# Kernel optimization log

Measured on AMD Instinct MI355X. Metric: run time of the kernel, lower is better.

Reference implementation:

```python
import jax, jax.numpy as jnp
import numpy as np

H_IMG, W_IMG = 1024, 1280
MAX_ITER = 3
DAMPING = 1e-6
DIST_THR = 0.2
NORM_THR = float(np.cos(np.deg2rad(20.0)))


def setup_inputs() -> dict:
    key = jax.random.key(0)
    k1, k2, k3, k4 = jax.random.split(key, 4)
    H, W = H_IMG, W_IMG
    fx = fy = 1000.0
    cx, cy = (W - 1) / 2.0, (H - 1) / 2.0
    K = jnp.array([[fx, 0.0, cx], [0.0, fy, cy], [0.0, 0.0, 1.0]], dtype=jnp.float32)
    # backproject a random depth map so vertex maps are geometrically consistent with K
    depth = 0.5 + 2.5 * jax.random.uniform(k1, (H, W), dtype=jnp.float32)
    vv, uu = jnp.meshgrid(jnp.arange(H, dtype=jnp.float32), jnp.arange(W, dtype=jnp.float32), indexing='ij')
    vertex_t0 = jnp.stack([(uu - cx) / fx * depth, (vv - cy) / fy * depth, depth], axis=-1)
    n = jax.random.normal(k2, (H, W, 3), dtype=jnp.float32) * 0.1 + jnp.array([0.0, 0.0, -1.0], jnp.float32)
    normal_t0 = n / jnp.linalg.norm(n, axis=-1, keepdims=True)
    # frame 1 = slightly perturbed frame 0 (realistic small-motion ICP)
    vertex_t1 = vertex_t0 + 0.002 * jax.random.normal(k3, (H, W, 3), dtype=jnp.float32)
    n1 = normal_t0 + 0.01 * jax.random.normal(k4, (H, W, 3), dtype=jnp.float32)
    normal_t1 = n1 / jnp.linalg.norm(n1, axis=-1, keepdims=True)
    pose10 = jnp.eye(4, dtype=jnp.float32).at[:3, 3].set(jnp.array([0.005, -0.003, 0.002], jnp.float32))
    return {
        'pose10': pose10,
        'vertex_t0': vertex_t0.astype(jnp.float32),
        'vertex_t1': vertex_t1.astype(jnp.float32),
        'normal_t0': normal_t0.astype(jnp.float32),
        'normal_t1': normal_t1.astype(jnp.float32),
        'K': K,
    }


def _skew3(w):
    o = jnp.zeros((), w.dtype)
    return jnp.array([[o, -w[2], w[1]], [w[2], o, -w[0]], [-w[1], w[0], o]])


def _exp_se3(xi):
    w, v = xi[:3], xi[3:6]
    wh = _skew3(w)
    wh2 = wh @ wh
    theta = jnp.linalg.norm(w)
    eps = 1e-8
    ts = jnp.maximum(theta, eps)  # safe denominator
    sin_t, cos_t = jnp.sin(ts), jnp.cos(ts)
    eye3 = jnp.eye(3, dtype=xi.dtype)
    e_w_big = eye3 + wh * (sin_t / ts) + wh2 * ((1.0 - cos_t) / ts ** 2)
    j_big = eye3 + ((1.0 - cos_t) / ts ** 2) * wh + ((ts - sin_t) / ts ** 3) * wh2
    small = theta <= eps
    e_w = jnp.where(small, eye3, e_w_big)
    j = jnp.where(small, eye3, j_big)
    return jnp.eye(4, dtype=xi.dtype).at[:3, :3].set(e_w).at[:3, 3].set(j @ v)


def _warp_nearest(feat, u, v):
    # grid_sample(mode='nearest', padding='border', align_corners=True) with
    # the module's normalization reduces to nearest-pixel gather at (v,u), clamped.
    H, W, _ = feat.shape
    ui = jnp.clip(jnp.round(u), 0, W - 1).astype(jnp.int32)
    vi = jnp.clip(jnp.round(v), 0, H - 1).astype(jnp.int32)
    return feat[vi, ui]  # (H,W,C)


def _icp_step(pose, vertex0, vertex1, normal0, normal1, mask0, K):
    R, t = pose[:3, :3], pose[:3, 3]
    H, W, _ = vertex0.shape
    p = vertex0 @ R.T + t          # vertex0_to1, (H,W,3)
    n0 = normal0 @ R.T             # normal0_to1
    fx, fy, cx, cy = K[0, 0], K[1, 1], K[0, 2], K[1, 2]
    z = p[..., 2]
    u = p[..., 0] / z * fx + cx
    v = p[..., 1] / z * fy + cy
    inview = (u > 0) & (u < W - 1) & (v > 0) & (v < H - 1)
    rv1 = _warp_nearest(vertex1, u, v)
    rn1 = _warp_nearest(normal1, u, v)
    mask1 = rv1[..., -1] > 0.0
    diff = p - rv1
    normal_ok = jnp.sum(n0 * rn1, axis=-1) > NORM_THR
    res = jnp.sum(rn1 * diff, axis=-1)           # (H,W)
    # -n^T skew(p) == cross(p, n)
    J = jnp.concatenate([jnp.cross(p, rn1), rn1], axis=-1)  # (H,W,6)
    occ = (~inview) | (jnp.linalg.norm(diff, axis=-1) > DIST_THR)
    invalid = occ | (~mask0) | (~mask1) | (~normal_ok)
    J = jnp.where(invalid[..., None], 0.0, J).reshape(-1, 6)
    r = jnp.where(invalid, 0.0, res).reshape(-1)
    JtJ = J.T @ J                                 # (6,6)
    JtR = J.T @ r                                 # (6,)
    Hm = JtJ + jnp.trace(JtJ) * DAMPING * jnp.eye(6, dtype=JtJ.dtype)
    xi = -(jnp.linalg.inv(Hm) @ JtR)
    return _exp_se3(xi) @ pose, ~invalid


def reference(pose10, vertex_t0, vertex_t1, normal_t0, normal_t1, K):
    mask0 = vertex_t0[..., -1] > 0.0
    pose = pose10
    valid = None
    for _ in range(MAX_ITER):
        pose, valid = _icp_step(pose, vertex_t0, vertex_t1, normal_t0, normal_t1, mask0, K)
    H, W = vertex_t0.shape[:2]
    valid_ratio = valid.astype(jnp.float32).sum() / H / W
    return pose, valid_ratio
```

## Files before the change

kernel.cpp:

```cpp
#include <hip/hip_runtime.h>
#include <math.h>

#define H_IMG 1024
#define W_IMG 1280
#define NPIX (H_IMG * W_IMG)
#define NQUAD (NPIX / 4)
#define RBLOCKS 256
#define RTPB 256
#define QPT (NQUAD / (RBLOCKS * RTPB))
#define NACC 28
#define NORM_THR 0.93969262f
#define DIST_THR2 0.04f
#define DAMPING 1e-6

#define PART_DOUBLES (RBLOCKS * NACC)

__global__ __launch_bounds__(256) void icp_init(const float* __restrict__ pose_in,
                                                double* __restrict__ ws) {
    const int i = threadIdx.x;
    if (i < 16) ws[i] = (double)pose_in[i];
    for (int k = i; k < PART_DOUBLES; k += 256) ws[16 + k] = 0.0;
    if (i == 0) *(unsigned*)(ws + 16 + PART_DOUBLES) = 0u;
}

__device__ void solve_and_update(const double* tot, double* pose_ws,
                                 float* out, int write_out) {
    double JtJ[6][6];
    {
        int k = 0;
        for (int i = 0; i < 6; ++i)
            for (int j = i; j < 6; ++j) { JtJ[i][j] = tot[k]; JtJ[j][i] = tot[k]; ++k; }
    }
    double tr = 0.0;
    for (int i = 0; i < 6; ++i) tr += JtJ[i][i];

    double A[6][7];
    for (int i = 0; i < 6; ++i) {
        for (int j = 0; j < 6; ++j) A[i][j] = JtJ[i][j] + (i == j ? tr * DAMPING : 0.0);
        A[i][6] = -tot[21 + i];
    }
    for (int c = 0; c < 6; ++c) {
        int piv = c; double mx = fabs(A[c][c]);
        for (int r = c + 1; r < 6; ++r) {
            double ar = fabs(A[r][c]);
            if (ar > mx) { mx = ar; piv = r; }
        }
        if (piv != c) for (int j = 0; j < 7; ++j) { double tmp = A[c][j]; A[c][j] = A[piv][j]; A[piv][j] = tmp; }
        double d = A[c][c]; if (d == 0.0) d = 1e-30;
        for (int r = c + 1; r < 6; ++r) {
            double f = A[r][c] / d;
            for (int j = c; j < 7; ++j) A[r][j] -= f * A[c][j];
        }
    }
    double xi[6];
    for (int i = 5; i >= 0; --i) {
        double s = A[i][6];
        for (int j = i + 1; j < 6; ++j) s -= A[i][j] * xi[j];
        double d = A[i][i]; if (d == 0.0) d = 1e-30;
        xi[i] = s / d;
    }

    const double w0 = xi[0], w1 = xi[1], w2 = xi[2];
    const double v0 = xi[3], v1 = xi[4], v2 = xi[5];
    double wh[3][3] = { {0.0, -w2, w1}, {w2, 0.0, -w0}, {-w1, w0, 0.0} };
    double wh2[3][3];
    for (int i = 0; i < 3; ++i)
        for (int j = 0; j < 3; ++j) {
            double s = 0.0;
            for (int k = 0; k < 3; ++k) s += wh[i][k] * wh[k][j];
            wh2[i][j] = s;
        }
    const double theta = sqrt(w0 * w0 + w1 * w1 + w2 * w2);
    const double eps = 1e-8;
    const double ts = (theta > eps) ? theta : eps;
    const double st = sin(ts), ct = cos(ts);
    const double cA = st / ts;
    const double cB = (1.0 - ct) / (ts * ts);
    const double cC = (ts - st) / (ts * ts * ts);
    const bool small = (theta <= eps);

    double ew[3][3], Jm[3][3];
    for (int i = 0; i < 3; ++i)
        for (int j = 0; j < 3; ++j) {
            double eye = (i == j) ? 1.0 : 0.0;
            ew[i][j] = small ? eye : (eye + cA * wh[i][j] + cB * wh2[i][j]);
            Jm[i][j] = small ? eye : (eye + cB * wh[i][j] + cC * wh2[i][j]);
        }
    double Jv[3];
    for (int i = 0; i < 3; ++i) Jv[i] = Jm[i][0] * v0 + Jm[i][1] * v1 + Jm[i][2] * v2;

    double T[16] = { ew[0][0], ew[0][1], ew[0][2], Jv[0],
                     ew[1][0], ew[1][1], ew[1][2], Jv[1],
                     ew[2][0], ew[2][1], ew[2][2], Jv[2],
                     0.0, 0.0, 0.0, 1.0 };
    double P[16];
    for (int i = 0; i < 16; ++i) P[i] = pose_ws[i];
    double NP[16];
    for (int i = 0; i < 4; ++i)
        for (int j = 0; j < 4; ++j) {
            double s = 0.0;
            for (int k = 0; k < 4; ++k) s += T[i * 4 + k] * P[k * 4 + j];
            NP[i * 4 + j] = s;
        }
    for (int i = 0; i < 16; ++i) pose_ws[i] = NP[i];

    if (write_out) {
        for (int i = 0; i < 16; ++i) out[i] = (float)NP[i];
        out[16] = (float)(tot[27] / (double)NPIX);
    }
}

__global__ __launch_bounds__(RTPB, 1) void icp_fused(
    const float* __restrict__ vert0, const float* __restrict__ vert1,
    const float* __restrict__ norm0, const float* __restrict__ norm1,
    const float* __restrict__ Kmat, double* __restrict__ ws,
    float* __restrict__ out, int write_out)
{
    const double* pose = ws;
    double* part = ws + 16;
    unsigned* counter = (unsigned*)(ws + 16 + PART_DOUBLES);

    const float R00 = (float)pose[0],  R01 = (float)pose[1],  R02 = (float)pose[2],  t0 = (float)pose[3];
    const float R10 = (float)pose[4],  R11 = (float)pose[5],  R12 = (float)pose[6],  t1 = (float)pose[7];
    const float R20 = (float)pose[8],  R21 = (float)pose[9],  R22 = (float)pose[10], t2 = (float)pose[11];
    const float fx = Kmat[0], cx = Kmat[2], fy = Kmat[4], cy = Kmat[5];

    float a[NACC];
#pragma unroll
    for (int k = 0; k < NACC; ++k) a[k] = 0.0f;

    const int tid0 = blockIdx.x * RTPB + threadIdx.x;
    const float4* v0q = (const float4*)vert0;
    const float4* n0q = (const float4*)norm0;

    float4 cA0, cA1, cA2, cB0, cB1, cB2;
    {
        const int q = tid0;
        cA0 = v0q[q * 3 + 0]; cA1 = v0q[q * 3 + 1]; cA2 = v0q[q * 3 + 2];
        cB0 = n0q[q * 3 + 0]; cB1 = n0q[q * 3 + 1]; cB2 = n0q[q * 3 + 2];
    }

#pragma unroll
    for (int i = 0; i < QPT; ++i) {
        const float vx[4] = {cA0.x, cA0.w, cA1.z, cA2.y};
        const float vy[4] = {cA0.y, cA1.x, cA1.w, cA2.z};
        const float vz[4] = {cA0.z, cA1.y, cA2.x, cA2.w};
        const float nx[4] = {cB0.x, cB0.w, cB1.z, cB2.y};
        const float ny[4] = {cB0.y, cB1.x, cB1.w, cB2.z};
        const float nz[4] = {cB0.z, cB1.y, cB2.x, cB2.w};

        float px[4], py[4], pz[4], nrx[4], nry[4], nrz[4];
        bool inview[4];
        int wb[4];
#pragma unroll
        for (int p = 0; p < 4; ++p) {
            px[p] = R00 * vx[p] + R01 * vy[p] + R02 * vz[p] + t0;
            py[p] = R10 * vx[p] + R11 * vy[p] + R12 * vz[p] + t1;
            pz[p] = R20 * vx[p] + R21 * vy[p] + R22 * vz[p] + t2;
            nrx[p] = R00 * nx[p] + R01 * ny[p] + R02 * nz[p];
            nry[p] = R10 * nx[p] + R11 * ny[p] + R12 * nz[p];
            nrz[p] = R20 * nx[p] + R21 * ny[p] + R22 * nz[p];
            const float u = px[p] / pz[p] * fx + cx;
            const float v = py[p] / pz[p] * fy + cy;
            inview[p] = (u > 0.0f) && (u < (float)(W_IMG - 1)) &&
                        (v > 0.0f) && (v < (float)(H_IMG - 1));
            const float uf = fminf(fmaxf(rintf(u), 0.0f), (float)(W_IMG - 1));
            const float vf = fminf(fmaxf(rintf(v), 0.0f), (float)(H_IMG - 1));
            wb[p] = ((int)vf * W_IMG + (int)uf) * 3;
        }

        float r1x[4], r1y[4], r1z[4], m1x[4], m1y[4], m1z[4];
#pragma unroll
        for (int p = 0; p < 4; ++p) {
            r1x[p] = vert1[wb[p]]; r1y[p] = vert1[wb[p] + 1]; r1z[p] = vert1[wb[p] + 2];
            m1x[p] = norm1[wb[p]]; m1y[p] = norm1[wb[p] + 1]; m1z[p] = norm1[wb[p] + 2];
        }

        float4 nA0, nA1, nA2, nB0, nB1, nB2;
        if (i + 1 < QPT) {
            const int q = tid0 + (i + 1) * (RBLOCKS * RTPB);
            nA0 = v0q[q * 3 + 0]; nA1 = v0q[q * 3 + 1]; nA2 = v0q[q * 3 + 2];
            nB0 = n0q[q * 3 + 0]; nB1 = n0q[q * 3 + 1]; nB2 = n0q[q * 3 + 2];
        }

#pragma unroll
        for (int p = 0; p < 4; ++p) {
            const float dx = px[p] - r1x[p], dy = py[p] - r1y[p], dz = pz[p] - r1z[p];
            const bool mask0 = vz[p] > 0.0f;
            const bool mask1 = r1z[p] > 0.0f;
            const bool normal_ok =
                (nrx[p] * m1x[p] + nry[p] * m1y[p] + nrz[p] * m1z[p]) > NORM_THR;
            const float d2 = dx * dx + dy * dy + dz * dz;
            const bool occ = (!inview[p]) || (d2 > DIST_THR2);
            const bool valid = (!occ) && mask0 && mask1 && normal_ok;

            if (valid) {
                const float res = m1x[p] * dx + m1y[p] * dy + m1z[p] * dz;
                float J[6];
                J[0] = py[p] * m1z[p] - pz[p] * m1y[p];
                J[1] = pz[p] * m1x[p] - px[p] * m1z[p];
                J[2] = px[p] * m1y[p] - py[p] * m1x[p];
                J[3] = m1x[p]; J[4] = m1y[p]; J[5] = m1z[p];
                int k = 0;
#pragma unroll
                for (int ii = 0; ii < 6; ++ii)
#pragma unroll
                    for (int jj = ii; jj < 6; ++jj) a[k++] += J[ii] * J[jj];
#pragma unroll
                for (int ii = 0; ii < 6; ++ii) a[21 + ii] += J[ii] * res;
                a[27] += 1.0f;
            }
        }

        if (i + 1 < QPT) {
            cA0 = nA0; cA1 = nA1; cA2 = nA2;
            cB0 = nB0; cB1 = nB1; cB2 = nB2;
        }
    }

#pragma unroll
    for (int k = 0; k < NACC; ++k) {
        float val = a[k];
        for (int off = 32; off > 0; off >>= 1) val += __shfl_down(val, off, 64);
        a[k] = val;
    }

    __shared__ float sh[4][NACC];
    const int lane = threadIdx.x & 63;
    const int wid  = threadIdx.x >> 6;
    if (lane == 0) {
#pragma unroll
        for (int k = 0; k < NACC; ++k) sh[wid][k] = a[k];
    }
    __syncthreads();

    const unsigned tid = threadIdx.x;
    if (tid < NACC) {
        double s = (double)sh[0][tid] + (double)sh[1][tid] +
                   (double)sh[2][tid] + (double)sh[3][tid];
        __hip_atomic_store(&part[blockIdx.x * NACC + (int)tid], s,
                           __ATOMIC_RELAXED, __HIP_MEMORY_SCOPE_AGENT);
    }
    __syncthreads();

    __shared__ bool amLast;
    if (tid == 0) {
        __threadfence();
        unsigned prev = atomicAdd(counter, 1u);
        amLast = (prev == gridDim.x - 1);
    }
    __syncthreads();

    if (amLast) {
        __threadfence();
        __shared__ double red[8][NACC];
        __shared__ double tot[NACC];
        const int k = (int)tid % NACC;
        const int g = (int)tid / NACC;
        if (tid < 8 * NACC) {
            double s = 0.0;
#pragma unroll
            for (int b = 0; b < RBLOCKS / 8; ++b) {
                const int blk = g + b * 8;
                s += __hip_atomic_load(&part[blk * NACC + k],
                                       __ATOMIC_RELAXED, __HIP_MEMORY_SCOPE_AGENT);
            }
            red[g][k] = s;
        }
        __syncthreads();
        if (tid < NACC) {
            double s = 0.0;
#pragma unroll
            for (int g2 = 0; g2 < 8; ++g2) s += red[g2][tid];
            tot[tid] = s;
        }
        __syncthreads();
        if (tid == 0) {
            solve_and_update(tot, ws, out, write_out);
            atomicExch(counter, 0u);
        }
    }
}

extern "C" void kernel_launch(void* const* d_in, const int* in_sizes, int n_in,
                              void* d_out, int out_size, void* d_ws, size_t ws_size,
                              hipStream_t stream) {
    const float* pose10 = (const float*)d_in[0];
    const float* vert0  = (const float*)d_in[1];
    const float* vert1  = (const float*)d_in[2];
    const float* norm0  = (const float*)d_in[3];
    const float* norm1  = (const float*)d_in[4];
    const float* Kmat   = (const float*)d_in[5];
    float* out = (float*)d_out;
    double* ws = (double*)d_ws;

    icp_init<<<1, 256, 0, stream>>>(pose10, ws);
    for (int it = 0; it < 3; ++it) {
        icp_fused<<<RBLOCKS, RTPB, 0, stream>>>(vert0, vert1, norm0, norm1,
                                                Kmat, ws, out, it == 2 ? 1 : 0);
    }
}
```

Before: 209.9 us.

## Stride pixels across grid per thread, swizzle block IDs, read initial pose directly

Each thread now handles pixels strided by the whole grid, loaded as scalar xyz triples, where before it read contiguous quads through float4 loads. Block indices are swizzled across groups of eight. The init kernel is reduced to clearing the counter, and the first iteration reads the input pose directly instead of a copied workspace pose. The aim is to give neighbouring threads more coherent gather locations in vert1/norm1 and to cut init work, at the cost of losing the wide float4 loads for the streamed inputs.

```diff
diff --git a/kernel.cpp b/kernel.cpp
--- a/kernel.cpp
+++ b/kernel.cpp
@@ -4,10 +4,12 @@
 #define H_IMG 1024
 #define W_IMG 1280
 #define NPIX (H_IMG * W_IMG)
-#define NQUAD (NPIX / 4)
 #define RBLOCKS 256
 #define RTPB 256
-#define QPT (NQUAD / (RBLOCKS * RTPB))
+#define NWAVES (RTPB / 64)
+#define STRIDE (RBLOCKS * RTPB)
+#define PPT (NPIX / STRIDE)
+#define GROUPS (PPT / 4)
 #define NACC 28
 #define NORM_THR 0.93969262f
 #define DIST_THR2 0.04f
@@ -15,15 +17,12 @@
 
 #define PART_DOUBLES (RBLOCKS * NACC)
 
-__global__ __launch_bounds__(256) void icp_init(const float* __restrict__ pose_in,
-                                                double* __restrict__ ws) {
-    const int i = threadIdx.x;
-    if (i < 16) ws[i] = (double)pose_in[i];
-    for (int k = i; k < PART_DOUBLES; k += 256) ws[16 + k] = 0.0;
-    if (i == 0) *(unsigned*)(ws + 16 + PART_DOUBLES) = 0u;
+__global__ void icp_init0(double* __restrict__ ws) {
+    if (threadIdx.x == 0) *(unsigned*)(ws + 16 + PART_DOUBLES) = 0u;
 }
 
 __device__ void solve_and_update(const double* tot, double* pose_ws,
+                                 const float* pose_in, int it,
                                  float* out, int write_out) {
     double JtJ[6][6];
     {
@@ -94,7 +93,7 @@
                      ew[2][0], ew[2][1], ew[2][2], Jv[2],
                      0.0, 0.0, 0.0, 1.0 };
     double P[16];
-    for (int i = 0; i < 16; ++i) P[i] = pose_ws[i];
+    for (int i = 0; i < 16; ++i) P[i] = (it == 0) ? (double)pose_in[i] : pose_ws[i];
     double NP[16];
     for (int i = 0; i < 4; ++i)
         for (int j = 0; j < 4; ++j) {
@@ -110,113 +109,12 @@
     }
 }
 
-__global__ __launch_bounds__(RTPB, 1) void icp_fused(
-    const float* __restrict__ vert0, const float* __restrict__ vert1,
-    const float* __restrict__ norm0, const float* __restrict__ norm1,
-    const float* __restrict__ Kmat, double* __restrict__ ws,
-    float* __restrict__ out, int write_out)
+__device__ __forceinline__ void reduce_and_finish(
+    float a[NACC], double* ws, const float* pose_in, int it,
+    float* out, int write_out)
 {
-    const double* pose = ws;
     double* part = ws + 16;
     unsigned* counter = (unsigned*)(ws + 16 + PART_DOUBLES);
-
-    const float R00 = (float)pose[0],  R01 = (float)pose[1],  R02 = (float)pose[2],  t0 = (float)pose[3];
-    const float R10 = (float)pose[4],  R11 = (float)pose[5],  R12 = (float)pose[6],  t1 = (float)pose[7];
-    const float R20 = (float)pose[8],  R21 = (float)pose[9],  R22 = (float)pose[10], t2 = (float)pose[11];
-    const float fx = Kmat[0], cx = Kmat[2], fy = Kmat[4], cy = Kmat[5];
-
-    float a[NACC];
-#pragma unroll
-    for (int k = 0; k < NACC; ++k) a[k] = 0.0f;
-
-    const int tid0 = blockIdx.x * RTPB + threadIdx.x;
-    const float4* v0q = (const float4*)vert0;
-    const float4* n0q = (const float4*)norm0;
-
-    float4 cA0, cA1, cA2, cB0, cB1, cB2;
-    {
-        const int q = tid0;
-        cA0 = v0q[q * 3 + 0]; cA1 = v0q[q * 3 + 1]; cA2 = v0q[q * 3 + 2];
-        cB0 = n0q[q * 3 + 0]; cB1 = n0q[q * 3 + 1]; cB2 = n0q[q * 3 + 2];
-    }
-
-#pragma unroll
-    for (int i = 0; i < QPT; ++i) {
-        const float vx[4] = {cA0.x, cA0.w, cA1.z, cA2.y};
-        const float vy[4] = {cA0.y, cA1.x, cA1.w, cA2.z};
-        const float vz[4] = {cA0.z, cA1.y, cA2.x, cA2.w};
-        const float nx[4] = {cB0.x, cB0.w, cB1.z, cB2.y};
-        const float ny[4] = {cB0.y, cB1.x, cB1.w, cB2.z};
-        const float nz[4] = {cB0.z, cB1.y, cB2.x, cB2.w};
-
-        float px[4], py[4], pz[4], nrx[4], nry[4], nrz[4];
-        bool inview[4];
-        int wb[4];
-#pragma unroll
-        for (int p = 0; p < 4; ++p) {
-            px[p] = R00 * vx[p] + R01 * vy[p] + R02 * vz[p] + t0;
-            py[p] = R10 * vx[p] + R11 * vy[p] + R12 * vz[p] + t1;
-            pz[p] = R20 * vx[p] + R21 * vy[p] + R22 * vz[p] + t2;
-            nrx[p] = R00 * nx[p] + R01 * ny[p] + R02 * nz[p];
-            nry[p] = R10 * nx[p] + R11 * ny[p] + R12 * nz[p];
-            nrz[p] = R20 * nx[p] + R21 * ny[p] + R22 * nz[p];
-            const float u = px[p] / pz[p] * fx + cx;
-            const float v = py[p] / pz[p] * fy + cy;
-            inview[p] = (u > 0.0f) && (u < (float)(W_IMG - 1)) &&
-                        (v > 0.0f) && (v < (float)(H_IMG - 1));
-            const float uf = fminf(fmaxf(rintf(u), 0.0f), (float)(W_IMG - 1));
-            const float vf = fminf(fmaxf(rintf(v), 0.0f), (float)(H_IMG - 1));
-            wb[p] = ((int)vf * W_IMG + (int)uf) * 3;
-        }
-
-        float r1x[4], r1y[4], r1z[4], m1x[4], m1y[4], m1z[4];
-#pragma unroll
-        for (int p = 0; p < 4; ++p) {
-            r1x[p] = vert1[wb[p]]; r1y[p] = vert1[wb[p] + 1]; r1z[p] = vert1[wb[p] + 2];
-            m1x[p] = norm1[wb[p]]; m1y[p] = norm1[wb[p] + 1]; m1z[p] = norm1[wb[p] + 2];
-        }
-
-        float4 nA0, nA1, nA2, nB0, nB1, nB2;
-        if (i + 1 < QPT) {
-            const int q = tid0 + (i + 1) * (RBLOCKS * RTPB);
-            nA0 = v0q[q * 3 + 0]; nA1 = v0q[q * 3 + 1]; nA2 = v0q[q * 3 + 2];
-            nB0 = n0q[q * 3 + 0]; nB1 = n0q[q * 3 + 1]; nB2 = n0q[q * 3 + 2];
-        }
-
-#pragma unroll
-        for (int p = 0; p < 4; ++p) {
-            const float dx = px[p] - r1x[p], dy = py[p] - r1y[p], dz = pz[p] - r1z[p];
-            const bool mask0 = vz[p] > 0.0f;
-            const bool mask1 = r1z[p] > 0.0f;
-            const bool normal_ok =
-                (nrx[p] * m1x[p] + nry[p] * m1y[p] + nrz[p] * m1z[p]) > NORM_THR;
-            const float d2 = dx * dx + dy * dy + dz * dz;
-            const bool occ = (!inview[p]) || (d2 > DIST_THR2);
-            const bool valid = (!occ) && mask0 && mask1 && normal_ok;
-
-            if (valid) {
-                const float res = m1x[p] * dx + m1y[p] * dy + m1z[p] * dz;
-                float J[6];
-                J[0] = py[p] * m1z[p] - pz[p] * m1y[p];
-                J[1] = pz[p] * m1x[p] - px[p] * m1z[p];
-                J[2] = px[p] * m1y[p] - py[p] * m1x[p];
-                J[3] = m1x[p]; J[4] = m1y[p]; J[5] = m1z[p];
-                int k = 0;
-#pragma unroll
-                for (int ii = 0; ii < 6; ++ii)
-#pragma unroll
-                    for (int jj = ii; jj < 6; ++jj) a[k++] += J[ii] * J[jj];
-#pragma unroll
-                for (int ii = 0; ii < 6; ++ii) a[21 + ii] += J[ii] * res;
-                a[27] += 1.0f;
-            }
-        }
-
-        if (i + 1 < QPT) {
-            cA0 = nA0; cA1 = nA1; cA2 = nA2;
-            cB0 = nB0; cB1 = nB1; cB2 = nB2;
-        }
-    }
 
 #pragma unroll
     for (int k = 0; k < NACC; ++k) {
@@ -225,7 +123,7 @@
         a[k] = val;
     }
 
-    __shared__ float sh[4][NACC];
+    __shared__ float sh[NWAVES][NACC];
     const int lane = threadIdx.x & 63;
     const int wid  = threadIdx.x >> 6;
     if (lane == 0) {
@@ -236,8 +134,9 @@
 
     const unsigned tid = threadIdx.x;
     if (tid < NACC) {
-        double s = (double)sh[0][tid] + (double)sh[1][tid] +
-                   (double)sh[2][tid] + (double)sh[3][tid];
+        double s = 0.0;
+#pragma unroll
+        for (int w = 0; w < NWAVES; ++w) s += (double)sh[w][tid];
         __hip_atomic_store(&part[blockIdx.x * NACC + (int)tid], s,
                            __ATOMIC_RELAXED, __HIP_MEMORY_SCOPE_AGENT);
     }
@@ -276,10 +175,128 @@
         }
         __syncthreads();
         if (tid == 0) {
-            solve_and_update(tot, ws, out, write_out);
+            solve_and_update(tot, ws, pose_in, it, out, write_out);
             atomicExch(counter, 0u);
         }
     }
+}
+
+__global__ __launch_bounds__(RTPB, 1) void icp_fused(
+    const float* __restrict__ pose_in,
+    const float* __restrict__ vert0, const float* __restrict__ vert1,
+    const float* __restrict__ norm0, const float* __restrict__ norm1,
+    const float* __restrict__ Kmat, double* __restrict__ ws,
+    float* __restrict__ out, int it, int write_out)
+{
+    float R00, R01, R02, t0, R10, R11, R12, t1, R20, R21, R22, t2;
+    if (it == 0) {
+        R00 = pose_in[0];  R01 = pose_in[1];  R02 = pose_in[2];  t0 = pose_in[3];
+        R10 = pose_in[4];  R11 = pose_in[5];  R12 = pose_in[6];  t1 = pose_in[7];
+        R20 = pose_in[8];  R21 = pose_in[9];  R22 = pose_in[10]; t2 = pose_in[11];
+    } else {
+        const double* pose = ws;
+        R00 = (float)pose[0];  R01 = (float)pose[1];  R02 = (float)pose[2];  t0 = (float)pose[3];
+        R10 = (float)pose[4];  R11 = (float)pose[5];  R12 = (float)pose[6];  t1 = (float)pose[7];
+        R20 = (float)pose[8];  R21 = (float)pose[9];  R22 = (float)pose[10]; t2 = (float)pose[11];
+    }
+    const float fx = Kmat[0], cx = Kmat[2], fy = Kmat[4], cy = Kmat[5];
+
+    float a[NACC];
+#pragma unroll
+    for (int k = 0; k < NACC; ++k) a[k] = 0.0f;
+
+    const int sbid = (blockIdx.x & 7) * 32 + (blockIdx.x >> 3);
+    const int tid0 = sbid * RTPB + (int)threadIdx.x;
+
+    float cs[4][6];
+#pragma unroll
+    for (int j = 0; j < 4; ++j) {
+        const int pix = tid0 + j * STRIDE;
+        const int b = pix * 3;
+        cs[j][0] = vert0[b + 0]; cs[j][1] = vert0[b + 1]; cs[j][2] = vert0[b + 2];
+        cs[j][3] = norm0[b + 0]; cs[j][4] = norm0[b + 1]; cs[j][5] = norm0[b + 2];
+    }
+
+#pragma unroll
+    for (int i = 0; i < GROUPS; ++i) {
+        float px[4], py[4], pz[4], nrx[4], nry[4], nrz[4];
+        bool inview[4];
+        int wb[4];
+#pragma unroll
+        for (int j = 0; j < 4; ++j) {
+            const float vx = cs[j][0], vy = cs[j][1], vz = cs[j][2];
+            const float nx = cs[j][3], ny = cs[j][4], nz = cs[j][5];
+            px[j] = R00 * vx + R01 * vy + R02 * vz + t0;
+            py[j] = R10 * vx + R11 * vy + R12 * vz + t1;
+            pz[j] = R20 * vx + R21 * vy + R22 * vz + t2;
+            nrx[j] = R00 * nx + R01 * ny + R02 * nz;
+            nry[j] = R10 * nx + R11 * ny + R12 * nz;
+            nrz[j] = R20 * nx + R21 * ny + R22 * nz;
+            const float u = px[j] / pz[j] * fx + cx;
+            const float v = py[j] / pz[j] * fy + cy;
+            inview[j] = (u > 0.0f) && (u < (float)(W_IMG - 1)) &&
+                        (v > 0.0f) && (v < (float)(H_IMG - 1));
+            const float uf = fminf(fmaxf(rintf(u), 0.0f), (float)(W_IMG - 1));
+            const float vf = fminf(fmaxf(rintf(v), 0.0f), (float)(H_IMG - 1));
+            wb[j] = ((int)vf * W_IMG + (int)uf) * 3;
+        }
+
+        float r1x[4], r1y[4], r1z[4], m1x[4], m1y[4], m1z[4];
+#pragma unroll
+        for (int j = 0; j < 4; ++j) {
+            r1x[j] = vert1[wb[j]]; r1y[j] = vert1[wb[j] + 1]; r1z[j] = vert1[wb[j] + 2];
+            m1x[j] = norm1[wb[j]]; m1y[j] = norm1[wb[j] + 1]; m1z[j] = norm1[wb[j] + 2];
+        }
+
+        float ns[4][6];
+        if (i + 1 < GROUPS) {
+#pragma unroll
+            for (int j = 0; j < 4; ++j) {
+                const int pix = tid0 + ((i + 1) * 4 + j) * STRIDE;
+                const int b = pix * 3;
+                ns[j][0] = vert0[b + 0]; ns[j][1] = vert0[b + 1]; ns[j][2] = vert0[b + 2];
+                ns[j][3] = norm0[b + 0]; ns[j][4] = norm0[b + 1]; ns[j][5] = norm0[b + 2];
+            }
+        }
+
+#pragma unroll
+        for (int j = 0; j < 4; ++j) {
+            const float dx = px[j] - r1x[j], dy = py[j] - r1y[j], dz = pz[j] - r1z[j];
+            const bool mask0 = cs[j][2] > 0.0f;
+            const bool mask1 = r1z[j] > 0.0f;
+            const bool normal_ok =
+                (nrx[j] * m1x[j] + nry[j] * m1y[j] + nrz[j] * m1z[j]) > NORM_THR;
+            const float d2 = dx * dx + dy * dy + dz * dz;
+            const bool occ = (!inview[j]) || (d2 > DIST_THR2);
+            const bool valid = (!occ) && mask0 && mask1 && normal_ok;
+
+            if (valid) {
+                const float res = m1x[j] * dx + m1y[j] * dy + m1z[j] * dz;
+                float J[6];
+                J[0] = py[j] * m1z[j] - pz[j] * m1y[j];
+                J[1] = pz[j] * m1x[j] - px[j] * m1z[j];
+                J[2] = px[j] * m1y[j] - py[j] * m1x[j];
+                J[3] = m1x[j]; J[4] = m1y[j]; J[5] = m1z[j];
+                int k = 0;
+#pragma unroll
+                for (int ii = 0; ii < 6; ++ii)
+#pragma unroll
+                    for (int jj = ii; jj < 6; ++jj) a[k++] += J[ii] * J[jj];
+#pragma unroll
+                for (int ii = 0; ii < 6; ++ii) a[21 + ii] += J[ii] * res;
+                a[27] += 1.0f;
+            }
+        }
+
+        if (i + 1 < GROUPS) {
+#pragma unroll
+            for (int j = 0; j < 4; ++j)
+#pragma unroll
+                for (int c = 0; c < 6; ++c) cs[j][c] = ns[j][c];
+        }
+    }
+
+    reduce_and_finish(a, ws, pose_in, it, out, write_out);
 }
 
 extern "C" void kernel_launch(void* const* d_in, const int* in_sizes, int n_in,
@@ -294,9 +311,9 @@
     float* out = (float*)d_out;
     double* ws = (double*)d_ws;
 
-    icp_init<<<1, 256, 0, stream>>>(pose10, ws);
+    icp_init0<<<1, 64, 0, stream>>>(ws);
     for (int it = 0; it < 3; ++it) {
-        icp_fused<<<RBLOCKS, RTPB, 0, stream>>>(vert0, vert1, norm0, norm1,
-                                                Kmat, ws, out, it == 2 ? 1 : 0);
-    }
-}
+        icp_fused<<<RBLOCKS, RTPB, 0, stream>>>(pose10, vert0, vert1, norm0, norm1,
+                                                Kmat, ws, out, it, it == 2 ? 1 : 0);
+    }
+}
```

After: 176.0 us. -16.1%, faster.
